# Performance work log

Measured on AMD Instinct MI355X. Metric: run time of the kernel, lower is better.

## Reference

```python
import jax, jax.numpy as jnp
import numpy as np

DIM = 1024
NUM_HEADS = 16
HEAD_DIM = DIM // NUM_HEADS
SCALE = HEAD_DIM ** -0.5


def setup_inputs() -> dict:
    key = jax.random.key(0)
    k_x, k_wqkv, k_bqkv, k_wp, k_bp = jax.random.split(key, 5)
    B, C, D = 4, 1024, DIM
    x = jax.random.normal(k_x, (B, C, D), dtype=jnp.float32)
    # nn.Linear stores weight as (out, in); we keep (in, out) for x @ W
    w_qkv = jax.random.normal(k_wqkv, (D, 3 * D), dtype=jnp.float32) * (D ** -0.5)
    b_qkv = jax.random.normal(k_bqkv, (3 * D,), dtype=jnp.float32) * 0.02
    w_proj = jax.random.normal(k_wp, (D, D), dtype=jnp.float32) * (D ** -0.5)
    b_proj = jax.random.normal(k_bp, (D,), dtype=jnp.float32) * 0.02
    return {"x": x, "w_qkv": w_qkv, "b_qkv": b_qkv, "w_proj": w_proj, "b_proj": b_proj}


def reference(x, w_qkv, b_qkv, w_proj, b_proj):
    B, C, D = x.shape
    H, Hd = NUM_HEADS, HEAD_DIM
    qkv = x @ w_qkv + b_qkv                       # (B, C, 3D)
    qkv = qkv.reshape(B, C, 3, H, Hd)
    q = qkv[:, :, 0].transpose(0, 2, 1, 3)        # (B, H, C, Hd)
    k = qkv[:, :, 1].transpose(0, 2, 1, 3)
    v = qkv[:, :, 2].transpose(0, 2, 1, 3)
    attn = jnp.einsum('bhqd,bhkd->bhqk', q, k) * SCALE
    attn = jax.nn.softmax(attn, axis=-1)
    out = jnp.einsum('bhqk,bhkd->bhqd', attn, v)  # (B, H, C, Hd)
    out = out.transpose(0, 2, 1, 3).reshape(B, C, D)
    return out @ w_proj + b_proj
```

## Files before the change

kernel.cpp:

```cpp
#include <hip/hip_runtime.h>
#include <cstdint>

#define BB 4
#define CC 1024
#define DD 1024
#define HH 16
#define HD 64
#define NH3 3072

typedef __attribute__((ext_vector_type(8))) short short8;
typedef __attribute__((ext_vector_type(4))) float f32x4;

#define MFMA16(a, b, c) __builtin_amdgcn_mfma_f32_16x16x32_bf16(a, b, c, 0, 0, 0)
#define EXP2 __builtin_amdgcn_exp2f

__device__ __forceinline__ void glds16(const void* g, void* l) {
    __builtin_amdgcn_global_load_lds(
        (const __attribute__((address_space(1))) void*)g,
        (__attribute__((address_space(3))) void*)l, 16, 0, 0);
}

__device__ __forceinline__ ushort f2bf(float f) {
    union { float f; uint32_t u; } v; v.f = f;
    uint32_t r = v.u + 0x7FFF + ((v.u >> 16) & 1);
    return (ushort)(r >> 16);
}

__device__ __forceinline__ uint32_t pack2bf(float a, float b) {
    uint32_t ua = __float_as_uint(a), ub = __float_as_uint(b);
    ua += 0x7FFF + ((ua >> 16) & 1);
    ub += 0x7FFF + ((ub >> 16) & 1);
    return __builtin_amdgcn_perm(ua, ub, 0x03020706);
}

__global__ __launch_bounds__(256)
void prep_kernel(const float* __restrict__ x, ushort* __restrict__ xbf,
                 const float* __restrict__ wqkv, ushort* __restrict__ wqkvT,
                 const float* __restrict__ wprj, ushort* __restrict__ wprjT)
{
    __shared__ float Ts[64 * 65];
    const int blk = blockIdx.x;
    const int t = threadIdx.x;

    if (blk < 4096) {
        int i = blk * 256 + t;
        float4 v = ((const float4*)x)[i];
        ushort4 o;
        o.x = f2bf(v.x); o.y = f2bf(v.y); o.z = f2bf(v.z); o.w = f2bf(v.w);
        ((ushort4*)xbf)[i] = o;
        return;
    }

    const float* in; ushort* outp; int K, N, n0, k0;
    if (blk < 4864) {
        int bx = blk - 4096;
        in = wqkv; outp = wqkvT; K = DD; N = NH3;
        n0 = (bx % 48) * 64; k0 = (bx / 48) * 64;
    } else {
        int bx = blk - 4864;
        in = wprj; outp = wprjT; K = DD; N = DD;
        n0 = (bx % 16) * 64; k0 = (bx / 16) * 64;
    }
    #pragma unroll
    for (int i = 0; i < 16; ++i) {
        int idx = t + i * 256;
        int r = idx >> 6, c = idx & 63;
        Ts[r * 65 + c] = in[(size_t)(k0 + r) * N + n0 + c];
    }
    __syncthreads();
    #pragma unroll
    for (int i = 0; i < 16; ++i) {
        int idx = t + i * 256;
        int rr = idx >> 6, cc = idx & 63;
        outp[(size_t)(n0 + rr) * K + k0 + cc] = f2bf(Ts[cc * 65 + rr]);
    }
}

template<int MODE, int MT>
__global__ __launch_bounds__(256)
void gemm_bt(const ushort* __restrict__ A, const ushort* __restrict__ Bt,
             const float* __restrict__ bias, float* __restrict__ Cf,
             ushort* __restrict__ qb, ushort* __restrict__ kb, ushort* __restrict__ vtb,
             int M, int N, int K)
{
    constexpr int MI = MT / 32;
    __shared__ ushort As[3][MT * 32];
    __shared__ ushort Bs[3][128 * 32];

    const int tid = threadIdx.x;
    const int wid = tid >> 6, lane = tid & 63;
    const int quad = lane >> 4, l15 = lane & 15;
    const int m0 = blockIdx.y * MT, n0 = blockIdx.x * 128;
    const int wm = (wid >> 1) * (MT / 2), wn = (wid & 1) * 64;

    const int sr = lane >> 2;
    const int sc = lane & 3;

    const int ar0 = wid * (MT / 4) + sr;
    const int acg0 = sc ^ ((ar0 >> 1) & 3);
    const int acg1 = sc ^ (((ar0 + 16) >> 1) & 3);
    const ushort* Ar0 = A + (size_t)(m0 + ar0) * K + acg0 * 8;
    const ushort* Ar1 = A + (size_t)(m0 + ar0 + 16) * K + acg1 * 8;
    const int br0 = wid * 32 + sr;
    const int bcg0 = sc ^ ((br0 >> 1) & 3);
    const int bcg1 = sc ^ (((br0 + 16) >> 1) & 3);
    const ushort* Br0 = Bt + (size_t)(n0 + br0) * K + bcg0 * 8;
    const ushort* Br1 = Bt + (size_t)(n0 + br0 + 16) * K + bcg1 * 8;

    f32x4 acc[MI][4];
    #pragma unroll
    for (int i = 0; i < MI; ++i)
        #pragma unroll
        for (int j = 0; j < 4; ++j) acc[i][j] = (f32x4)(0.0f);

#define GSTAGE(kn, bidx) do { \
        glds16(Ar0 + (kn), &As[bidx][(wid * (MT / 4)) * 32]); \
        glds16(Br0 + (kn), &Bs[bidx][(wid * 32) * 32]); \
        if (MT == 128) glds16(Ar1 + (kn), &As[bidx][(wid * 32 + 16) * 32]); \
        glds16(Br1 + (kn), &Bs[bidx][(wid * 32 + 16) * 32]); } while (0)

    GSTAGE(0, 0);
    GSTAGE(32, 1);

    int cur = 0;
    for (int k0 = 0; k0 < K; k0 += 32) {
        if (k0 + 32 < K) {
            if (MT == 128)
                asm volatile("s_waitcnt vmcnt(4)\n\ts_barrier" ::: "memory");
            else
                asm volatile("s_waitcnt vmcnt(3)\n\ts_barrier" ::: "memory");
        } else {
            asm volatile("s_waitcnt vmcnt(0)\n\ts_barrier" ::: "memory");
        }
        if (k0 + 64 < K) {
            const int nb = (cur >= 1) ? cur - 1 : 2;
            GSTAGE(k0 + 64, nb);
        }

        short8 af[MI], bf[4];
        #pragma unroll
        for (int i = 0; i < MI; ++i) {
            int row = wm + i * 16 + l15;
            af[i] = *(const short8*)(&As[cur][row * 32 + (quad ^ ((row >> 1) & 3)) * 8]);
        }
        #pragma unroll
        for (int j = 0; j < 4; ++j) {
            int col = wn + j * 16 + l15;
            bf[j] = *(const short8*)(&Bs[cur][col * 32 + (quad ^ ((col >> 1) & 3)) * 8]);
        }
        #pragma unroll
        for (int i = 0; i < MI; ++i)
            #pragma unroll
            for (int j = 0; j < 4; ++j)
                acc[i][j] = MFMA16(af[i], bf[j], acc[i][j]);

        cur = (cur == 2) ? 0 : cur + 1;
    }
#undef GSTAGE

    if (MODE == 0) {
        #pragma unroll
        for (int i = 0; i < MI; ++i) {
            int row = m0 + wm + i * 16 + quad * 4;
            #pragma unroll
            for (int j = 0; j < 4; ++j) {
                int col = n0 + wn + j * 16 + l15;
                float bv = bias[col];
                #pragma unroll
                for (int r = 0; r < 4; ++r)
                    Cf[(size_t)(row + r) * N + col] = acc[i][j][r] + bv;
            }
        }
    } else {
        #pragma unroll
        for (int j = 0; j < 4; ++j) {
            int n = n0 + wn + j * 16 + l15;
            int three = n >> 10;
            int h = (n >> 6) & 15;
            int hd = n & 63;
            float scale = (three == 0) ? 0.1803368801f : 1.0f;
            float bv = bias[n];
            #pragma unroll
            for (int i = 0; i < MI; ++i) {
                int row = m0 + wm + i * 16 + quad * 4;
                #pragma unroll
                for (int r = 0; r < 4; ++r) {
                    int m = row + r;
                    int b = m >> 10, c = m & 1023;
                    ushort val = f2bf((acc[i][j][r] + bv) * scale);
                    if (three == 0)
                        qb[((size_t)((b * HH + h) * CC) + c) * HD + hd] = val;
                    else if (three == 1)
                        kb[((size_t)((b * HH + h) * CC) + c) * HD + hd] = val;
                    else
                        vtb[((size_t)((b * HH + h) * HD) + hd) * CC + c] = val;
                }
            }
        }
    }
}

__device__ __forceinline__ short8 pvfrag(const uint32_t pk0[2], const uint32_t pk1[2],
                                         int quad, int l15) {
    union { short8 s; uint32_t u[4]; } r;
    #pragma unroll
    for (int w = 0; w < 4; ++w) {
        int src = ((quad & 1) * 2 + (w >> 1)) * 16 + l15;
        uint32_t v0 = (uint32_t)__shfl((int)pk0[w & 1], src);
        uint32_t v1 = (uint32_t)__shfl((int)pk1[w & 1], src);
        r.u[w] = (quad < 2) ? v0 : v1;
    }
    return r.s;
}

__global__ __launch_bounds__(256)
void attn_mfma7(const ushort* __restrict__ qb, const ushort* __restrict__ kb,
                const ushort* __restrict__ vt, ushort* __restrict__ attnb)
{
    __shared__ ushort lds[3 * 4096 + 4 * 4096];
    const uint K0 = 0, K1 = 4096, K2 = 8192;
    const uint V0 = 12288, V1 = 16384, V2 = 20480, V3 = 24576;

    const int tid = threadIdx.x;
    const int wid = tid >> 6, lane = tid & 63;
    const int quad = lane >> 4, l15 = lane & 15;
    const int bh = blockIdx.x & 63;
    const int qt = blockIdx.x >> 6;
    const int q0 = qt * 128;
    const int b = bh >> 4, h = bh & 15;

    const ushort* Qp  = qb + ((size_t)bh * CC + q0) * HD;
    const ushort* Kp  = kb + (size_t)bh * CC * HD;
    const ushort* Vtp = vt + (size_t)bh * HD * CC;

    const int sr = lane >> 3;
    const int sc = lane & 7;

    short8 qf[2][2];
    #pragma unroll
    for (int q2 = 0; q2 < 2; ++q2) {
        int row = wid * 32 + q2 * 16 + l15;
        #pragma unroll
        for (int s = 0; s < 2; ++s)
            qf[q2][s] = *(const short8*)(Qp + (size_t)row * HD + (s * 4 + quad) * 8);
    }

    const int kr = wid * 16 + sr;
    const int cgA = sc ^ (kr & 7);
    const int cgB = sc ^ ((kr + 8) & 7);
    const ushort* Kr0 = Kp  + (size_t)kr * HD + cgA * 8;
    const ushort* Kr1 = Kp  + (size_t)(kr + 8) * HD + cgB * 8;
    const ushort* Vr0 = Vtp + (size_t)kr * CC + cgA * 8;
    const ushort* Vr1 = Vtp + (size_t)(kr + 8) * CC + cgB * 8;

    const uint stg0 = (wid * 16) * 64;
    const uint stg1 = (wid * 16 + 8) * 64;

    glds16(Kr0, lds + K0 + stg0);
    glds16(Kr1, lds + K0 + stg1);
    glds16(Vr0, lds + V0 + stg0);
    glds16(Vr1, lds + V0 + stg1);
    glds16(Kr0 + (size_t)64 * HD, lds + K1 + stg0);
    glds16(Kr1 + (size_t)64 * HD, lds + K1 + stg1);
    glds16(Vr0 + 64, lds + V1 + stg0);
    glds16(Vr1 + 64, lds + V1 + stg1);

    f32x4 oacc[2][4];
    #pragma unroll
    for (int q2 = 0; q2 < 2; ++q2)
        #pragma unroll
        for (int hb = 0; hb < 4; ++hb) oacc[q2][hb] = (f32x4)(0.0f);
    float lsum[2] = {0.0f, 0.0f};

    uint ksC = K0, ksN = K1, ksF = K2;
    uint vsP = V3, vsC = V0, vsN = V1, vsF = V2;

    uint32_t pkA[2][4][2], pkB[2][4][2];
    #pragma unroll
    for (int q2 = 0; q2 < 2; ++q2)
        #pragma unroll
        for (int kb2 = 0; kb2 < 4; ++kb2)
            pkA[q2][kb2][0] = pkA[q2][kb2][1] = 0u;

#define APV(PKP) do { \
        short8 vf_[4][2]; \
        _Pragma("unroll") \
        for (int hb = 0; hb < 4; ++hb) { \
            int hr = hb * 16 + l15; \
            vf_[hb][0] = *(const short8*)(lds + vsP + hr * 64 + ((quad ^ (hr & 7)) * 8)); \
            vf_[hb][1] = *(const short8*)(lds + vsP + hr * 64 + (((4 + quad) ^ (hr & 7)) * 8)); \
        } \
        short8 pf_[2][2]; \
        _Pragma("unroll") \
        for (int q2 = 0; q2 < 2; ++q2) { \
            pf_[q2][0] = pvfrag(PKP[q2][0], PKP[q2][1], quad, l15); \
            pf_[q2][1] = pvfrag(PKP[q2][2], PKP[q2][3], quad, l15); \
        } \
        __builtin_amdgcn_s_setprio(1); \
        _Pragma("unroll") \
        for (int q2 = 0; q2 < 2; ++q2) \
            _Pragma("unroll") \
            for (int hb = 0; hb < 4; ++hb) { \
                oacc[q2][hb] = MFMA16(pf_[q2][0], vf_[hb][0], oacc[q2][hb]); \
                oacc[q2][hb] = MFMA16(pf_[q2][1], vf_[hb][1], oacc[q2][hb]); \
            } \
        __builtin_amdgcn_s_setprio(0); \
    } while (0)

#define AITER(kt, PKP, PKC) do { \
        if ((kt) < 15) asm volatile("s_waitcnt vmcnt(4)\n\ts_barrier" ::: "memory"); \
        else           asm volatile("s_waitcnt vmcnt(0)\n\ts_barrier" ::: "memory"); \
        if ((kt) < 14) {                      \
            const int koff_ = ((kt) + 2) * 64; \
            glds16(Kr0 + (size_t)koff_ * HD, lds + ksF + stg0); \
            glds16(Kr1 + (size_t)koff_ * HD, lds + ksF + stg1); \
            glds16(Vr0 + koff_,              lds + vsF + stg0); \
            glds16(Vr1 + koff_,              lds + vsF + stg1); \
        } \
        if ((kt) > 0) APV(PKP); \
         \
        _Pragma("unroll") \
        for (int kb2 = 0; kb2 < 4; ++kb2) { \
            int krow_ = kb2 * 16 + l15; \
            short8 kf0_ = *(const short8*)(lds + ksC + krow_ * 64 + ((quad ^ (krow_ & 7)) * 8)); \
            short8 kf1_ = *(const short8*)(lds + ksC + krow_ * 64 + (((4 + quad) ^ (krow_ & 7)) * 8)); \
            _Pragma("unroll") \
            for (int q2 = 0; q2 < 2; ++q2) { \
                f32x4 st_ = (f32x4)(0.0f); \
                st_ = MFMA16(kf0_, qf[q2][0], st_); \
                st_ = MFMA16(kf1_, qf[q2][1], st_); \
                float p0_ = EXP2(st_[0]); \
                float p1_ = EXP2(st_[1]); \
                float p2_ = EXP2(st_[2]); \
                float p3_ = EXP2(st_[3]); \
                lsum[q2] += (p0_ + p1_) + (p2_ + p3_); \
                PKC[q2][kb2][0] = pack2bf(p0_, p1_); \
                PKC[q2][kb2][1] = pack2bf(p2_, p3_); \
            } \
        } \
         \
        uint t_ = ksC; ksC = ksN; ksN = ksF; ksF = t_; \
        t_ = vsP; vsP = vsC; vsC = vsN; vsN = vsF; vsF = t_; \
    } while (0)

    for (int k2 = 0; k2 < 8; ++k2) {
        AITER(2 * k2,     pkA, pkB);
        AITER(2 * k2 + 1, pkB, pkA);
    }

    APV(pkA);
#undef AITER
#undef APV

    #pragma unroll
    for (int q2 = 0; q2 < 2; ++q2) {
        lsum[q2] += __shfl_xor(lsum[q2], 16);
        lsum[q2] += __shfl_xor(lsum[q2], 32);
    }

    #pragma unroll
    for (int q2 = 0; q2 < 2; ++q2) {
        #pragma unroll
        for (int r = 0; r < 4; ++r) {
            float inv = 1.0f / __shfl(lsum[q2], (lane & 48) | (quad * 4 + r));
            int c = q0 + wid * 32 + q2 * 16 + quad * 4 + r;
            #pragma unroll
            for (int hb = 0; hb < 4; ++hb) {
                int d = h * 64 + hb * 16 + l15;
                attnb[((size_t)(b * CC + c)) * DD + d] = f2bf(oacc[q2][hb][r] * inv);
            }
        }
    }
}

extern "C" void kernel_launch(void* const* d_in, const int* in_sizes, int n_in,
                              void* d_out, int out_size, void* d_ws, size_t ws_size,
                              hipStream_t stream)
{
    (void)in_sizes; (void)n_in; (void)out_size; (void)ws_size;
    const float* x      = (const float*)d_in[0];
    const float* w_qkv  = (const float*)d_in[1];
    const float* b_qkv  = (const float*)d_in[2];
    const float* w_proj = (const float*)d_in[3];
    const float* b_proj = (const float*)d_in[4];
    float* out = (float*)d_out;

    ushort* p = (ushort*)d_ws;
    ushort* xbf   = p;  p += (size_t)4 * 1024 * 1024;
    ushort* wqkvT = p;  p += (size_t)3 * 1024 * 1024;
    ushort* wprjT = p;  p += (size_t)1 * 1024 * 1024;
    ushort* qbuf  = p;  p += (size_t)4 * 1024 * 1024;
    ushort* kbuf  = p;  p += (size_t)4 * 1024 * 1024;
    ushort* vtb   = p;  p += (size_t)4 * 1024 * 1024;
    ushort* attnb = p;  p += (size_t)4 * 1024 * 1024;

    prep_kernel<<<5120, 256, 0, stream>>>(x, xbf, w_qkv, wqkvT, w_proj, wprjT);

    gemm_bt<1, 128><<<dim3(NH3 / 128, (BB * CC) / 128), 256, 0, stream>>>(
        xbf, wqkvT, b_qkv, nullptr, qbuf, kbuf, vtb, BB * CC, NH3, DD);

    attn_mfma7<<<512, 256, 0, stream>>>(qbuf, kbuf, vtb, attnb);

    gemm_bt<0, 64><<<dim3(DD / 128, (BB * CC) / 64), 256, 0, stream>>>(
        attnb, wprjT, b_proj, out, nullptr, nullptr, nullptr, BB * CC, DD, DD);
}
```

Before: 178.8 us.

## Stage softmax probabilities through LDS and add XCD-aware block swizzle to GEMMs

The attention kernel now writes the bf16 probability tile into a padded LDS region and reads it back as MFMA A-operand fragments. This replaces the cross-lane shuffle-based fragment rebuild and the pkA/pkB register double-buffer. Both GEMM launches use a 1D grid remapped so that consecutive tiles land on the same XCD, which is meant to improve L2 reuse. In exchange, attention LDS use grows by about 18 KB per block and each iteration adds extra LDS write/read traffic.

Result: faster. 174.5 us (-2.4%).

```diff
diff --git a/kernel.cpp b/kernel.cpp
--- a/kernel.cpp
+++ b/kernel.cpp
@@ -76,7 +76,7 @@
     }
 }
 
-template<int MODE, int MT>
+template<int MODE, int MT, int SWZ>
 __global__ __launch_bounds__(256)
 void gemm_bt(const ushort* __restrict__ A, const ushort* __restrict__ Bt,
              const float* __restrict__ bias, float* __restrict__ Cf,
@@ -90,7 +90,18 @@
     const int tid = threadIdx.x;
     const int wid = tid >> 6, lane = tid & 63;
     const int quad = lane >> 4, l15 = lane & 15;
-    const int m0 = blockIdx.y * MT, n0 = blockIdx.x * 128;
+
+    int bxi, byi;
+    if (SWZ) {
+        const int flat = blockIdx.x;
+        const int cpx = gridDim.x >> 3;
+        const int f2 = (flat & 7) * cpx + (flat >> 3);
+        const int nbx = N / 128;
+        bxi = f2 % nbx; byi = f2 / nbx;
+    } else {
+        bxi = blockIdx.x; byi = blockIdx.y;
+    }
+    const int m0 = byi * MT, n0 = bxi * 128;
     const int wm = (wid >> 1) * (MT / 2), wn = (wid & 1) * 64;
 
     const int sr = lane >> 2;
@@ -200,26 +211,14 @@
     }
 }
 
-__device__ __forceinline__ short8 pvfrag(const uint32_t pk0[2], const uint32_t pk1[2],
-                                         int quad, int l15) {
-    union { short8 s; uint32_t u[4]; } r;
-    #pragma unroll
-    for (int w = 0; w < 4; ++w) {
-        int src = ((quad & 1) * 2 + (w >> 1)) * 16 + l15;
-        uint32_t v0 = (uint32_t)__shfl((int)pk0[w & 1], src);
-        uint32_t v1 = (uint32_t)__shfl((int)pk1[w & 1], src);
-        r.u[w] = (quad < 2) ? v0 : v1;
-    }
-    return r.s;
-}
-
 __global__ __launch_bounds__(256)
-void attn_mfma7(const ushort* __restrict__ qb, const ushort* __restrict__ kb,
+void attn_mfma8(const ushort* __restrict__ qb, const ushort* __restrict__ kb,
                 const ushort* __restrict__ vt, ushort* __restrict__ attnb)
 {
-    __shared__ ushort lds[3 * 4096 + 4 * 4096];
+    __shared__ ushort lds[3 * 4096 + 4 * 4096 + 9216];
     const uint K0 = 0, K1 = 4096, K2 = 8192;
     const uint V0 = 12288, V1 = 16384, V2 = 20480, V3 = 24576;
+    const uint P0 = 28672;
 
     const int tid = threadIdx.x;
     const int wid = tid >> 6, lane = tid & 63;
@@ -275,14 +274,7 @@
     uint ksC = K0, ksN = K1, ksF = K2;
     uint vsP = V3, vsC = V0, vsN = V1, vsF = V2;
 
-    uint32_t pkA[2][4][2], pkB[2][4][2];
-    #pragma unroll
-    for (int q2 = 0; q2 < 2; ++q2)
-        #pragma unroll
-        for (int kb2 = 0; kb2 < 4; ++kb2)
-            pkA[q2][kb2][0] = pkA[q2][kb2][1] = 0u;
-
-#define APV(PKP) do { \
+#define APV() do { \
         short8 vf_[4][2]; \
         _Pragma("unroll") \
         for (int hb = 0; hb < 4; ++hb) { \
@@ -290,66 +282,61 @@
             vf_[hb][0] = *(const short8*)(lds + vsP + hr * 64 + ((quad ^ (hr & 7)) * 8)); \
             vf_[hb][1] = *(const short8*)(lds + vsP + hr * 64 + (((4 + quad) ^ (hr & 7)) * 8)); \
         } \
-        short8 pf_[2][2]; \
         _Pragma("unroll") \
         for (int q2 = 0; q2 < 2; ++q2) { \
-            pf_[q2][0] = pvfrag(PKP[q2][0], PKP[q2][1], quad, l15); \
-            pf_[q2][1] = pvfrag(PKP[q2][2], PKP[q2][3], quad, l15); \
-        } \
-        __builtin_amdgcn_s_setprio(1); \
-        _Pragma("unroll") \
-        for (int q2 = 0; q2 < 2; ++q2) \
+            int row = wid * 32 + q2 * 16 + l15; \
+            short8 pf0 = *(const short8*)(lds + P0 + row * 72 + quad * 8); \
+            short8 pf1 = *(const short8*)(lds + P0 + row * 72 + 32 + quad * 8); \
+            __builtin_amdgcn_s_setprio(1); \
             _Pragma("unroll") \
             for (int hb = 0; hb < 4; ++hb) { \
-                oacc[q2][hb] = MFMA16(pf_[q2][0], vf_[hb][0], oacc[q2][hb]); \
-                oacc[q2][hb] = MFMA16(pf_[q2][1], vf_[hb][1], oacc[q2][hb]); \
+                oacc[q2][hb] = MFMA16(pf0, vf_[hb][0], oacc[q2][hb]); \
+                oacc[q2][hb] = MFMA16(pf1, vf_[hb][1], oacc[q2][hb]); \
             } \
-        __builtin_amdgcn_s_setprio(0); \
+            __builtin_amdgcn_s_setprio(0); \
+        } \
     } while (0)
 
-#define AITER(kt, PKP, PKC) do { \
-        if ((kt) < 15) asm volatile("s_waitcnt vmcnt(4)\n\ts_barrier" ::: "memory"); \
-        else           asm volatile("s_waitcnt vmcnt(0)\n\ts_barrier" ::: "memory"); \
-        if ((kt) < 14) {                      \
-            const int koff_ = ((kt) + 2) * 64; \
-            glds16(Kr0 + (size_t)koff_ * HD, lds + ksF + stg0); \
-            glds16(Kr1 + (size_t)koff_ * HD, lds + ksF + stg1); \
-            glds16(Vr0 + koff_,              lds + vsF + stg0); \
-            glds16(Vr1 + koff_,              lds + vsF + stg1); \
-        } \
-        if ((kt) > 0) APV(PKP); \
-         \
-        _Pragma("unroll") \
-        for (int kb2 = 0; kb2 < 4; ++kb2) { \
-            int krow_ = kb2 * 16 + l15; \
-            short8 kf0_ = *(const short8*)(lds + ksC + krow_ * 64 + ((quad ^ (krow_ & 7)) * 8)); \
-            short8 kf1_ = *(const short8*)(lds + ksC + krow_ * 64 + (((4 + quad) ^ (krow_ & 7)) * 8)); \
-            _Pragma("unroll") \
-            for (int q2 = 0; q2 < 2; ++q2) { \
-                f32x4 st_ = (f32x4)(0.0f); \
-                st_ = MFMA16(kf0_, qf[q2][0], st_); \
-                st_ = MFMA16(kf1_, qf[q2][1], st_); \
-                float p0_ = EXP2(st_[0]); \
-                float p1_ = EXP2(st_[1]); \
-                float p2_ = EXP2(st_[2]); \
-                float p3_ = EXP2(st_[3]); \
-                lsum[q2] += (p0_ + p1_) + (p2_ + p3_); \
-                PKC[q2][kb2][0] = pack2bf(p0_, p1_); \
-                PKC[q2][kb2][1] = pack2bf(p2_, p3_); \
-            } \
-        } \
-         \
-        uint t_ = ksC; ksC = ksN; ksN = ksF; ksF = t_; \
-        t_ = vsP; vsP = vsC; vsC = vsN; vsN = vsF; vsF = t_; \
-    } while (0)
-
-    for (int k2 = 0; k2 < 8; ++k2) {
-        AITER(2 * k2,     pkA, pkB);
-        AITER(2 * k2 + 1, pkB, pkA);
-    }
-
-    APV(pkA);
-#undef AITER
+    for (int kt = 0; kt < 16; ++kt) {
+        if (kt < 15) asm volatile("s_waitcnt vmcnt(4)\n\ts_barrier" ::: "memory");
+        else         asm volatile("s_waitcnt vmcnt(0)\n\ts_barrier" ::: "memory");
+
+        if (kt < 14) {
+            const int koff = (kt + 2) * 64;
+            glds16(Kr0 + (size_t)koff * HD, lds + ksF + stg0);
+            glds16(Kr1 + (size_t)koff * HD, lds + ksF + stg1);
+            glds16(Vr0 + koff,              lds + vsF + stg0);
+            glds16(Vr1 + koff,              lds + vsF + stg1);
+        }
+
+        if (kt > 0) APV();
+
+        #pragma unroll
+        for (int kb2 = 0; kb2 < 4; ++kb2) {
+            int krow = kb2 * 16 + l15;
+            short8 kf0 = *(const short8*)(lds + ksC + krow * 64 + ((quad ^ (krow & 7)) * 8));
+            short8 kf1 = *(const short8*)(lds + ksC + krow * 64 + (((4 + quad) ^ (krow & 7)) * 8));
+            #pragma unroll
+            for (int q2 = 0; q2 < 2; ++q2) {
+                f32x4 st = (f32x4)(0.0f);
+                st = MFMA16(kf0, qf[q2][0], st);
+                st = MFMA16(kf1, qf[q2][1], st);
+                float p0 = EXP2(st[0]);
+                float p1 = EXP2(st[1]);
+                float p2 = EXP2(st[2]);
+                float p3 = EXP2(st[3]);
+                lsum[q2] += (p0 + p1) + (p2 + p3);
+                int row = wid * 32 + q2 * 16 + l15;
+                *(uint2*)(lds + P0 + row * 72 + kb2 * 16 + quad * 4) =
+                    make_uint2(pack2bf(p0, p1), pack2bf(p2, p3));
+            }
+        }
+
+        uint t = ksC; ksC = ksN; ksN = ksF; ksF = t;
+        t = vsP; vsP = vsC; vsC = vsN; vsN = vsF; vsF = t;
+    }
+
+    APV();
 #undef APV
 
     #pragma unroll
@@ -396,11 +383,11 @@
 
     prep_kernel<<<5120, 256, 0, stream>>>(x, xbf, w_qkv, wqkvT, w_proj, wprjT);
 
-    gemm_bt<1, 128><<<dim3(NH3 / 128, (BB * CC) / 128), 256, 0, stream>>>(
+    gemm_bt<1, 128, 1><<<768, 256, 0, stream>>>(
         xbf, wqkvT, b_qkv, nullptr, qbuf, kbuf, vtb, BB * CC, NH3, DD);
 
-    attn_mfma7<<<512, 256, 0, stream>>>(qbuf, kbuf, vtb, attnb);
-
-    gemm_bt<0, 64><<<dim3(DD / 128, (BB * CC) / 64), 256, 0, stream>>>(
+    attn_mfma8<<<512, 256, 0, stream>>>(qbuf, kbuf, vtb, attnb);
+
+    gemm_bt<0, 64, 1><<<512, 256, 0, stream>>>(
         attnb, wprjT, b_proj, out, nullptr, nullptr, nullptr, BB * CC, DD, DD);
 }
```

## Switch attention to 32x32 MFMA with permlane P reshuffle; swizzle proj GEMM grid

Applied to the files above, without the earlier changes.

Rewrites the attention kernel to use 32x32x16 bf16 MFMA tiles for both QK^T and PV, holding Q as four fragments per lane and replacing the shuffle-based P-fragment rebuild with v_permlane32_swap. This cuts the number of MFMA issues, the LDS fragment reads and the cross-lane shuffles per tile, and simplifies the row-sum reduction. It also launches the output-projection GEMM as a flat 1-D grid with an XCD-style block remap intended to improve L2 locality. The risks are higher register pressure from 16-wide accumulators and a subtle fragment-layout mapping that has to match the MFMA operand layout.

Result: faster. 172.0 us (-3.8%).

```diff
diff --git a/kernel.cpp b/kernel.cpp
--- a/kernel.cpp
+++ b/kernel.cpp
@@ -10,8 +10,10 @@
 
 typedef __attribute__((ext_vector_type(8))) short short8;
 typedef __attribute__((ext_vector_type(4))) float f32x4;
+typedef __attribute__((ext_vector_type(16))) float f32x16;
 
 #define MFMA16(a, b, c) __builtin_amdgcn_mfma_f32_16x16x32_bf16(a, b, c, 0, 0, 0)
+#define MFMA32(a, b, c) __builtin_amdgcn_mfma_f32_32x32x16_bf16(a, b, c, 0, 0, 0)
 #define EXP2 __builtin_amdgcn_exp2f
 
 __device__ __forceinline__ void glds16(const void* g, void* l) {
@@ -76,7 +78,7 @@
     }
 }
 
-template<int MODE, int MT>
+template<int MODE, int MT, int SWZ>
 __global__ __launch_bounds__(256)
 void gemm_bt(const ushort* __restrict__ A, const ushort* __restrict__ Bt,
              const float* __restrict__ bias, float* __restrict__ Cf,
@@ -90,7 +92,18 @@
     const int tid = threadIdx.x;
     const int wid = tid >> 6, lane = tid & 63;
     const int quad = lane >> 4, l15 = lane & 15;
-    const int m0 = blockIdx.y * MT, n0 = blockIdx.x * 128;
+
+    int bxi, byi;
+    if (SWZ) {
+        const int flat = blockIdx.x;
+        const int cpx = gridDim.x >> 3;
+        const int f2 = (flat & 7) * cpx + (flat >> 3);
+        const int nbx = N / 128;
+        bxi = f2 % nbx; byi = f2 / nbx;
+    } else {
+        bxi = blockIdx.x; byi = blockIdx.y;
+    }
+    const int m0 = byi * MT, n0 = bxi * 128;
     const int wm = (wid >> 1) * (MT / 2), wn = (wid & 1) * 64;
 
     const int sr = lane >> 2;
@@ -200,21 +213,8 @@
     }
 }
 
-__device__ __forceinline__ short8 pvfrag(const uint32_t pk0[2], const uint32_t pk1[2],
-                                         int quad, int l15) {
-    union { short8 s; uint32_t u[4]; } r;
-    #pragma unroll
-    for (int w = 0; w < 4; ++w) {
-        int src = ((quad & 1) * 2 + (w >> 1)) * 16 + l15;
-        uint32_t v0 = (uint32_t)__shfl((int)pk0[w & 1], src);
-        uint32_t v1 = (uint32_t)__shfl((int)pk1[w & 1], src);
-        r.u[w] = (quad < 2) ? v0 : v1;
-    }
-    return r.s;
-}
-
 __global__ __launch_bounds__(256)
-void attn_mfma7(const ushort* __restrict__ qb, const ushort* __restrict__ kb,
+void attn_mfma9(const ushort* __restrict__ qb, const ushort* __restrict__ kbuf,
                 const ushort* __restrict__ vt, ushort* __restrict__ attnb)
 {
     __shared__ ushort lds[3 * 4096 + 4 * 4096];
@@ -223,28 +223,26 @@
 
     const int tid = threadIdx.x;
     const int wid = tid >> 6, lane = tid & 63;
-    const int quad = lane >> 4, l15 = lane & 15;
+    const int l31 = lane & 31, hi = lane >> 5;
     const int bh = blockIdx.x & 63;
     const int qt = blockIdx.x >> 6;
     const int q0 = qt * 128;
     const int b = bh >> 4, h = bh & 15;
 
-    const ushort* Qp  = qb + ((size_t)bh * CC + q0) * HD;
-    const ushort* Kp  = kb + (size_t)bh * CC * HD;
-    const ushort* Vtp = vt + (size_t)bh * HD * CC;
+    const ushort* Qp  = qb  + ((size_t)bh * CC + q0) * HD;
+    const ushort* Kp  = kbuf + (size_t)bh * CC * HD;
+    const ushort* Vtp = vt  + (size_t)bh * HD * CC;
+
+    short8 qf[4];
+    {
+        const int qrow = wid * 32 + l31;
+        #pragma unroll
+        for (int s = 0; s < 4; ++s)
+            qf[s] = *(const short8*)(Qp + (size_t)qrow * HD + s * 16 + hi * 8);
+    }
 
     const int sr = lane >> 3;
     const int sc = lane & 7;
-
-    short8 qf[2][2];
-    #pragma unroll
-    for (int q2 = 0; q2 < 2; ++q2) {
-        int row = wid * 32 + q2 * 16 + l15;
-        #pragma unroll
-        for (int s = 0; s < 2; ++s)
-            qf[q2][s] = *(const short8*)(Qp + (size_t)row * HD + (s * 4 + quad) * 8);
-    }
-
     const int kr = wid * 16 + sr;
     const int cgA = sc ^ (kr & 7);
     const int cgB = sc ^ ((kr + 8) & 7);
@@ -265,49 +263,39 @@
     glds16(Vr0 + 64, lds + V1 + stg0);
     glds16(Vr1 + 64, lds + V1 + stg1);
 
-    f32x4 oacc[2][4];
-    #pragma unroll
-    for (int q2 = 0; q2 < 2; ++q2)
-        #pragma unroll
-        for (int hb = 0; hb < 4; ++hb) oacc[q2][hb] = (f32x4)(0.0f);
-    float lsum[2] = {0.0f, 0.0f};
+    f32x16 oacc[2];
+    oacc[0] = (f32x16)(0.0f);
+    oacc[1] = (f32x16)(0.0f);
+    float lsum = 0.0f;
 
     uint ksC = K0, ksN = K1, ksF = K2;
     uint vsP = V3, vsC = V0, vsN = V1, vsF = V2;
 
-    uint32_t pkA[2][4][2], pkB[2][4][2];
-    #pragma unroll
-    for (int q2 = 0; q2 < 2; ++q2)
-        #pragma unroll
-        for (int kb2 = 0; kb2 < 4; ++kb2)
-            pkA[q2][kb2][0] = pkA[q2][kb2][1] = 0u;
-
-#define APV(PKP) do { \
-        short8 vf_[4][2]; \
-        _Pragma("unroll") \
-        for (int hb = 0; hb < 4; ++hb) { \
-            int hr = hb * 16 + l15; \
-            vf_[hb][0] = *(const short8*)(lds + vsP + hr * 64 + ((quad ^ (hr & 7)) * 8)); \
-            vf_[hb][1] = *(const short8*)(lds + vsP + hr * 64 + (((4 + quad) ^ (hr & 7)) * 8)); \
-        } \
-        short8 pf_[2][2]; \
-        _Pragma("unroll") \
-        for (int q2 = 0; q2 < 2; ++q2) { \
-            pf_[q2][0] = pvfrag(PKP[q2][0], PKP[q2][1], quad, l15); \
-            pf_[q2][1] = pvfrag(PKP[q2][2], PKP[q2][3], quad, l15); \
-        } \
+    uint32_t pkA[2][8], pkB[2][8];
+
+#define APV9(PKP) do { \
         __builtin_amdgcn_s_setprio(1); \
         _Pragma("unroll") \
-        for (int q2 = 0; q2 < 2; ++q2) \
+        for (int m = 0; m < 4; ++m) { \
+            const int kb2_ = m >> 1, s4_ = (m & 1) * 4; \
+            uint32_t x0_ = PKP[kb2_][s4_ + 0], x1_ = PKP[kb2_][s4_ + 1]; \
+            uint32_t y0_ = PKP[kb2_][s4_ + 2], y1_ = PKP[kb2_][s4_ + 3]; \
+            asm("v_permlane32_swap_b32 %0, %1" : "+v"(x0_), "+v"(y0_)); \
+            asm("v_permlane32_swap_b32 %0, %1" : "+v"(x1_), "+v"(y1_)); \
+            union { short8 s; uint32_t u[4]; } pu_; \
+            pu_.u[0] = x0_; pu_.u[1] = x1_; pu_.u[2] = y0_; pu_.u[3] = y1_; \
             _Pragma("unroll") \
-            for (int hb = 0; hb < 4; ++hb) { \
-                oacc[q2][hb] = MFMA16(pf_[q2][0], vf_[hb][0], oacc[q2][hb]); \
-                oacc[q2][hb] = MFMA16(pf_[q2][1], vf_[hb][1], oacc[q2][hb]); \
+            for (int db_ = 0; db_ < 2; ++db_) { \
+                int hr_ = db_ * 32 + l31; \
+                short8 vf_ = *(const short8*)(lds + vsP + hr_ * 64 + \
+                                (((m * 2 + hi) ^ (hr_ & 7)) * 8)); \
+                oacc[db_] = MFMA32(pu_.s, vf_, oacc[db_]); \
             } \
+        } \
         __builtin_amdgcn_s_setprio(0); \
     } while (0)
 
-#define AITER(kt, PKP, PKC) do { \
+#define AITER9(kt, PKP, PKC) do { \
         if ((kt) < 15) asm volatile("s_waitcnt vmcnt(4)\n\ts_barrier" ::: "memory"); \
         else           asm volatile("s_waitcnt vmcnt(0)\n\ts_barrier" ::: "memory"); \
         if ((kt) < 14) {                      \
@@ -317,25 +305,29 @@
             glds16(Vr0 + koff_,              lds + vsF + stg0); \
             glds16(Vr1 + koff_,              lds + vsF + stg1); \
         } \
-        if ((kt) > 0) APV(PKP); \
+        if ((kt) > 0) { APV9(PKP); } \
          \
         _Pragma("unroll") \
-        for (int kb2 = 0; kb2 < 4; ++kb2) { \
-            int krow_ = kb2 * 16 + l15; \
-            short8 kf0_ = *(const short8*)(lds + ksC + krow_ * 64 + ((quad ^ (krow_ & 7)) * 8)); \
-            short8 kf1_ = *(const short8*)(lds + ksC + krow_ * 64 + (((4 + quad) ^ (krow_ & 7)) * 8)); \
+        for (int kb2 = 0; kb2 < 2; ++kb2) { \
+            f32x16 sacc = (f32x16)(0.0f); \
             _Pragma("unroll") \
-            for (int q2 = 0; q2 < 2; ++q2) { \
-                f32x4 st_ = (f32x4)(0.0f); \
-                st_ = MFMA16(kf0_, qf[q2][0], st_); \
-                st_ = MFMA16(kf1_, qf[q2][1], st_); \
-                float p0_ = EXP2(st_[0]); \
-                float p1_ = EXP2(st_[1]); \
-                float p2_ = EXP2(st_[2]); \
-                float p3_ = EXP2(st_[3]); \
-                lsum[q2] += (p0_ + p1_) + (p2_ + p3_); \
-                PKC[q2][kb2][0] = pack2bf(p0_, p1_); \
-                PKC[q2][kb2][1] = pack2bf(p2_, p3_); \
+            for (int s = 0; s < 4; ++s) { \
+                int row = kb2 * 32 + l31; \
+                short8 kf = *(const short8*)(lds + ksC + row * 64 + \
+                                (((s * 2 + hi) ^ (row & 7)) * 8)); \
+                sacc = MFMA32(kf, qf[s], sacc); \
+            } \
+            float p_[16]; \
+            _Pragma("unroll") \
+            for (int r = 0; r < 16; ++r) p_[r] = EXP2(sacc[r]); \
+            lsum += ((((p_[0] + p_[1]) + (p_[2] + p_[3])) + \
+                      ((p_[4] + p_[5]) + (p_[6] + p_[7]))) + \
+                     (((p_[8] + p_[9]) + (p_[10] + p_[11])) + \
+                      ((p_[12] + p_[13]) + (p_[14] + p_[15])))); \
+            _Pragma("unroll") \
+            for (int g = 0; g < 4; ++g) { \
+                PKC[kb2][2 * g]     = pack2bf(p_[4 * g],     p_[4 * g + 1]); \
+                PKC[kb2][2 * g + 1] = pack2bf(p_[4 * g + 2], p_[4 * g + 3]); \
             } \
         } \
          \
@@ -344,31 +336,25 @@
     } while (0)
 
     for (int k2 = 0; k2 < 8; ++k2) {
-        AITER(2 * k2,     pkA, pkB);
-        AITER(2 * k2 + 1, pkB, pkA);
-    }
-
-    APV(pkA);
-#undef AITER
-#undef APV
+        AITER9(2 * k2,     pkA, pkB);
+        AITER9(2 * k2 + 1, pkB, pkA);
+    }
+
+    APV9(pkA);
+#undef AITER9
+#undef APV9
+
+    lsum += __shfl_xor(lsum, 32);
 
     #pragma unroll
-    for (int q2 = 0; q2 < 2; ++q2) {
-        lsum[q2] += __shfl_xor(lsum[q2], 16);
-        lsum[q2] += __shfl_xor(lsum[q2], 32);
-    }
-
-    #pragma unroll
-    for (int q2 = 0; q2 < 2; ++q2) {
-        #pragma unroll
-        for (int r = 0; r < 4; ++r) {
-            float inv = 1.0f / __shfl(lsum[q2], (lane & 48) | (quad * 4 + r));
-            int c = q0 + wid * 32 + q2 * 16 + quad * 4 + r;
-            #pragma unroll
-            for (int hb = 0; hb < 4; ++hb) {
-                int d = h * 64 + hb * 16 + l15;
-                attnb[((size_t)(b * CC + c)) * DD + d] = f2bf(oacc[q2][hb][r] * inv);
-            }
+    for (int r = 0; r < 16; ++r) {
+        int qm = (r & 3) + 8 * (r >> 2) + 4 * hi;
+        float inv = 1.0f / __shfl(lsum, qm);
+        int c = q0 + wid * 32 + qm;
+        #pragma unroll
+        for (int dblk = 0; dblk < 2; ++dblk) {
+            int d = h * 64 + dblk * 32 + l31;
+            attnb[((size_t)(b * CC + c)) * DD + d] = f2bf(oacc[dblk][r] * inv);
         }
     }
 }
@@ -396,11 +382,11 @@
 
     prep_kernel<<<5120, 256, 0, stream>>>(x, xbf, w_qkv, wqkvT, w_proj, wprjT);
 
-    gemm_bt<1, 128><<<dim3(NH3 / 128, (BB * CC) / 128), 256, 0, stream>>>(
+    gemm_bt<1, 128, 0><<<dim3(NH3 / 128, (BB * CC) / 128), 256, 0, stream>>>(
         xbf, wqkvT, b_qkv, nullptr, qbuf, kbuf, vtb, BB * CC, NH3, DD);
 
-    attn_mfma7<<<512, 256, 0, stream>>>(qbuf, kbuf, vtb, attnb);
-
-    gemm_bt<0, 64><<<dim3(DD / 128, (BB * CC) / 64), 256, 0, stream>>>(
+    attn_mfma9<<<512, 256, 0, stream>>>(qbuf, kbuf, vtb, attnb);
+
+    gemm_bt<0, 64, 1><<<512, 256, 0, stream>>>(
         attnb, wprjT, b_proj, out, nullptr, nullptr, nullptr, BB * CC, DD, DD);
 }
```
